# Kernel tuning notes

Measured on AMD Instinct MI355X. Metric: run time of the kernel, lower is better.

Reference implementation:

```python
import jax, jax.numpy as jnp
import numpy as np

EMBED, HEADS, FF, WIN = 512, 8, 2048, 64
SIGMA, PSTRENGTH, PERIOD, THRESH = 2.0, 1.0, 100.0, 0.0


def layer_norm(x, g, b, eps=1e-5):
    mu = jnp.mean(x, axis=-1, keepdims=True)
    var = jnp.var(x, axis=-1, keepdims=True)
    return (x - mu) * jax.lax.rsqrt(var + eps) * g + b


def setup_inputs() -> dict:
    key = jax.random.key(0)
    ks = jax.random.split(key, 16)
    s = 1.0 / np.sqrt(EMBED)
    sf = 1.0 / np.sqrt(FF)
    inp = {
        "src": jax.random.normal(ks[0], (8, 2048, EMBED), dtype=jnp.float32),
        "Wq": jax.random.normal(ks[1], (EMBED, EMBED), dtype=jnp.float32) * s,
        "bq": jnp.zeros((EMBED,), jnp.float32),
        "Wk": jax.random.normal(ks[2], (EMBED, EMBED), dtype=jnp.float32) * s,
        "bk": jnp.zeros((EMBED,), jnp.float32),
        "Wv": jax.random.normal(ks[3], (EMBED, EMBED), dtype=jnp.float32) * s,
        "bv": jnp.zeros((EMBED,), jnp.float32),
        "Wo": jax.random.normal(ks[4], (EMBED, EMBED), dtype=jnp.float32) * s,
        "bo": jnp.zeros((EMBED,), jnp.float32),
        "Wg": jax.random.normal(ks[5], (EMBED, 1), dtype=jnp.float32) * s,
        "bg": jnp.zeros((1,), jnp.float32),
        "W1": jax.random.normal(ks[6], (EMBED, FF), dtype=jnp.float32) * s,
        "b1": jnp.zeros((FF,), jnp.float32),
        "W2": jax.random.normal(ks[7], (FF, EMBED), dtype=jnp.float32) * sf,
        "b2": jnp.zeros((EMBED,), jnp.float32),
        "ln1_g": jnp.ones((EMBED,), jnp.float32),
        "ln1_b": jnp.zeros((EMBED,), jnp.float32),
        "ln2_g": jnp.ones((EMBED,), jnp.float32),
        "ln2_b": jnp.zeros((EMBED,), jnp.float32),
    }
    return inp


def gated_sparse_attn(x, Wq, bq, Wk, bk, Wv, bv, Wo, bo, Wg, bg):
    B, S, D = x.shape
    H, dh = HEADS, D // HEADS
    q = (x @ Wq + bq).reshape(B, S, H, dh).transpose(0, 2, 1, 3)  # [B,H,S,dh]
    k = (x @ Wk + bk).reshape(B, S, H, dh).transpose(0, 2, 1, 3)
    v = (x @ Wv + bv).reshape(B, S, H, dh).transpose(0, 2, 1, 3)
    scores = jnp.einsum('bhqd,bhkd->bhqk', q, k) / jnp.sqrt(jnp.float32(dh))
    idx = jnp.arange(S, dtype=jnp.float32)
    dist = idx[:, None] - idx[None, :]  # [S,S]
    gauss_bias = jnp.exp(-(dist * dist) / (2.0 * SIGMA * SIGMA))
    per_bias = PSTRENGTH * jnp.cos(2.0 * jnp.pi * dist / PERIOD)
    scores = scores + gauss_bias + per_bias  # positional biases baked into scores
    local = jnp.abs(dist) <= WIN  # local-window sparsity mask
    scores = jnp.where(local, scores, jnp.float32(-1e9))
    attn = jax.nn.softmax(scores, axis=-1)
    out = jnp.einsum('bhqk,bhkd->bhqd', attn, v)
    out = out.transpose(0, 2, 1, 3).reshape(B, S, D) @ Wo + bo
    gate = jax.nn.sigmoid(x @ Wg + bg)  # [B,S,1] learned gating
    gate = jnp.where(gate > THRESH, gate, jnp.float32(0.0))
    return gate * out


def reference(src, Wq, bq, Wk, bk, Wv, bv, Wo, bo, Wg, bg, W1, b1, W2, b2, ln1_g, ln1_b, ln2_g, ln2_b):
    # dropout is identity in eval mode
    attn_out = gated_sparse_attn(src, Wq, bq, Wk, bk, Wv, bv, Wo, bo, Wg, bg)
    x = layer_norm(src + attn_out, ln1_g, ln1_b)
    ff = jax.nn.relu(x @ W1 + b1) @ W2 + b2
    return layer_norm(x + ff, ln2_g, ln2_b)
```

## Files before the change

### kernel.cpp

```cpp
#include <hip/hip_runtime.h>
#include <hip/hip_bf16.h>
#include <math.h>

#define S_LEN   2048
#define D_MOD   512
#define N_HEADS 8
#define D_HEAD  64
#define FF_DIM  2048
#define M_ROWS  16384
#define BHSD    8388608

typedef __attribute__((ext_vector_type(8))) __bf16 bf16x8;
typedef __attribute__((ext_vector_type(4))) float  f32x4;
typedef unsigned short u16;

__device__ __forceinline__ u16 f2bf(float f) {
  unsigned u = __float_as_uint(f);
  u += 0x7fffu + ((u >> 16) & 1u);
  return (u16)(u >> 16);
}
__device__ __forceinline__ float bf2f(u16 h) { return __uint_as_float(((unsigned)h) << 16); }

__device__ __forceinline__ f32x4 mfma16(bf16x8 a, bf16x8 b, f32x4 c) {
  return __builtin_amdgcn_mfma_f32_16x16x32_bf16(a, b, c, 0, 0, 0);
}

__device__ __forceinline__ void async16(void* lds, const void* g) {
  __builtin_amdgcn_global_load_lds(
      (const __attribute__((address_space(1))) unsigned int*)g,
      (__attribute__((address_space(3))) unsigned int*)lds, 16, 0, 0);
}

#define BAR()    asm volatile("s_barrier" ::: "memory")
#define WAITV(n) asm volatile("s_waitcnt vmcnt(" #n ")" ::: "memory")
#define WAITL()  asm volatile("s_waitcnt lgkmcnt(0)" ::: "memory")

__device__ __forceinline__ int swz384(int row, int bir) {
  return row * 384 + ((bir & ~127) | ((bir ^ ((row & 7) << 4)) & 127));
}

__global__ __launch_bounds__(256) void cvt_gate(const float* __restrict__ src,
                                                const float* __restrict__ Wg,
                                                const float* __restrict__ bg,
                                                u16* __restrict__ xb,
                                                float* __restrict__ gate) {
  const int wid = threadIdx.x >> 6, lane = threadIdx.x & 63;
  const size_t row = (size_t)blockIdx.x * 4 + wid;
  const float4* s = reinterpret_cast<const float4*>(src + row * D_MOD);
  const float4* w = reinterpret_cast<const float4*>(Wg);
  float4 a0 = s[lane * 2], a1 = s[lane * 2 + 1];
  float4 w0 = w[lane * 2], w1 = w[lane * 2 + 1];
  float acc = a0.x * w0.x + a0.y * w0.y + a0.z * w0.z + a0.w * w0.w +
              a1.x * w1.x + a1.y * w1.y + a1.z * w1.z + a1.w * w1.w;
#pragma unroll
  for (int m = 1; m < 64; m <<= 1) acc += __shfl_xor(acc, m);
  ushort4 h0, h1;
  h0.x = f2bf(a0.x); h0.y = f2bf(a0.y); h0.z = f2bf(a0.z); h0.w = f2bf(a0.w);
  h1.x = f2bf(a1.x); h1.y = f2bf(a1.y); h1.z = f2bf(a1.z); h1.w = f2bf(a1.w);
  ushort4* ob = reinterpret_cast<ushort4*>(xb + row * D_MOD);
  ob[lane * 2] = h0; ob[lane * 2 + 1] = h1;
  if (lane == 0) {
    float g = 1.f / (1.f + __expf(-(acc + bg[0])));
    gate[row] = g > 0.f ? g : 0.f;
  }
}

__global__ void transpose_cvt(const float* __restrict__ in, u16* __restrict__ out,
                              int K, int N) {
  __shared__ float t[32][33];
  const int n0 = blockIdx.x * 32, k0 = blockIdx.y * 32;
  const int tx = threadIdx.x, ty = threadIdx.y;
#pragma unroll
  for (int i = 0; i < 4; ++i)
    t[ty + 8 * i][tx] = in[(size_t)(k0 + ty + 8 * i) * N + n0 + tx];
  __syncthreads();
#pragma unroll
  for (int i = 0; i < 4; ++i)
    out[(size_t)(n0 + ty + 8 * i) * K + k0 + tx] = f2bf(t[tx][ty + 8 * i]);
}

__global__ __launch_bounds__(256) void vtr_k(const u16* __restrict__ V,
                                             u16* __restrict__ VT) {
  __shared__ __align__(16) u16 T[64 * 64];
  const int tid = threadIdx.x;
  const int wid = tid >> 6, lane = tid & 63;
  const int bh = blockIdx.y;
  const int s0 = blockIdx.x * 64;
  const u16* Vb = V + ((size_t)bh * S_LEN + s0) * D_HEAD;
#pragma unroll
  for (int r = 0; r < 2; ++r) {
    const int c = r * 256 + tid;
    const int s = c >> 3;
    const int blk = (c & 7) ^ ((s >> 3) & 7);
    async16((char*)T + (r * 4 + wid) * 1024, Vb + (size_t)s * D_HEAD + blk * 8);
  }
  __syncthreads();
  u16* VTb = VT + (size_t)bh * D_HEAD * S_LEN;
#pragma unroll
  for (int r = 0; r < 2; ++r) {
    const int d  = (r * 4 + wid) * 8 + (lane >> 3);
    const int s8 = lane & 7;
    ushort4 w0, w1;
    u16 tmp[8];
#pragma unroll
    for (int j = 0; j < 8; ++j) {
      const int s = s8 * 8 + j;
      tmp[j] = *reinterpret_cast<const u16*>(
          (const char*)T + s * 128 + ((2 * d) ^ (((s >> 3) & 7) << 4)));
    }
    w0.x = tmp[0]; w0.y = tmp[1]; w0.z = tmp[2]; w0.w = tmp[3];
    w1.x = tmp[4]; w1.y = tmp[5]; w1.z = tmp[6]; w1.w = tmp[7];
    ushort4* dst = reinterpret_cast<ushort4*>(VTb + (size_t)d * S_LEN + s0 + s8 * 8);
    dst[0] = w0; dst[1] = w1;
  }
}

__global__ __launch_bounds__(256) void ln1red_k(const u16* __restrict__ xb,
                                                const float* __restrict__ gate,
                                                const u16* __restrict__ p0,
                                                const u16* __restrict__ p1,
                                                const float* __restrict__ bo,
                                                const float* __restrict__ gam,
                                                const float* __restrict__ bet,
                                                u16* __restrict__ outb) {
  const int wid = threadIdx.x >> 6, lane = threadIdx.x & 63;
  const size_t row = (size_t)blockIdx.x * 4 + wid;
  const size_t base = row * D_MOD;
  const float g = gate[row];
  const ushort4* sp = reinterpret_cast<const ushort4*>(xb + base);
  const ushort4* a  = reinterpret_cast<const ushort4*>(p0 + base);
  const ushort4* c  = reinterpret_cast<const ushort4*>(p1 + base);
  const float4*  bb = reinterpret_cast<const float4*>(bo);
  ushort4 s0 = sp[lane * 2], s1 = sp[lane * 2 + 1];
  ushort4 a0 = a[lane * 2], a1 = a[lane * 2 + 1];
  ushort4 c0 = c[lane * 2], c1 = c[lane * 2 + 1];
  float4 d0 = bb[lane * 2], d1 = bb[lane * 2 + 1];
  float4 v0, v1;
  v0.x = bf2f(s0.x) + g * (bf2f(a0.x) + bf2f(c0.x) + d0.x);
  v0.y = bf2f(s0.y) + g * (bf2f(a0.y) + bf2f(c0.y) + d0.y);
  v0.z = bf2f(s0.z) + g * (bf2f(a0.z) + bf2f(c0.z) + d0.z);
  v0.w = bf2f(s0.w) + g * (bf2f(a0.w) + bf2f(c0.w) + d0.w);
  v1.x = bf2f(s1.x) + g * (bf2f(a1.x) + bf2f(c1.x) + d1.x);
  v1.y = bf2f(s1.y) + g * (bf2f(a1.y) + bf2f(c1.y) + d1.y);
  v1.z = bf2f(s1.z) + g * (bf2f(a1.z) + bf2f(c1.z) + d1.z);
  v1.w = bf2f(s1.w) + g * (bf2f(a1.w) + bf2f(c1.w) + d1.w);
  float s  = v0.x + v0.y + v0.z + v0.w + v1.x + v1.y + v1.z + v1.w;
  float s2 = v0.x * v0.x + v0.y * v0.y + v0.z * v0.z + v0.w * v0.w +
             v1.x * v1.x + v1.y * v1.y + v1.z * v1.z + v1.w * v1.w;
#pragma unroll
  for (int m = 1; m < 64; m <<= 1) { s += __shfl_xor(s, m); s2 += __shfl_xor(s2, m); }
  const float mu = s * (1.0f / 512.0f);
  const float var = s2 * (1.0f / 512.0f) - mu * mu;
  const float rs = 1.0f / sqrtf(var + 1e-5f);
  const float4* gp = reinterpret_cast<const float4*>(gam);
  const float4* bp = reinterpret_cast<const float4*>(bet);
  float4 g0 = gp[lane * 2], g1 = gp[lane * 2 + 1];
  float4 e0 = bp[lane * 2], e1 = bp[lane * 2 + 1];
  ushort4 h0, h1;
  h0.x = f2bf((v0.x - mu) * rs * g0.x + e0.x);  h0.y = f2bf((v0.y - mu) * rs * g0.y + e0.y);
  h0.z = f2bf((v0.z - mu) * rs * g0.z + e0.z);  h0.w = f2bf((v0.w - mu) * rs * g0.w + e0.w);
  h1.x = f2bf((v1.x - mu) * rs * g1.x + e1.x);  h1.y = f2bf((v1.y - mu) * rs * g1.y + e1.y);
  h1.z = f2bf((v1.z - mu) * rs * g1.z + e1.z);  h1.w = f2bf((v1.w - mu) * rs * g1.w + e1.w);
  ushort4* ob = reinterpret_cast<ushort4*>(outb + base);
  ob[lane * 2] = h0; ob[lane * 2 + 1] = h1;
}

__global__ __launch_bounds__(256) void ln2red_k(const u16* __restrict__ xb,
                                                const u16* __restrict__ p0,
                                                const u16* __restrict__ p1,
                                                const float* __restrict__ b2,
                                                const float* __restrict__ gam,
                                                const float* __restrict__ bet,
                                                float* __restrict__ out) {
  const int wid = threadIdx.x >> 6, lane = threadIdx.x & 63;
  const size_t row = (size_t)blockIdx.x * 4 + wid;
  const size_t base = row * D_MOD;
  const ushort4* xp = reinterpret_cast<const ushort4*>(xb + base);
  const ushort4* q0 = reinterpret_cast<const ushort4*>(p0 + base);
  const ushort4* q1 = reinterpret_cast<const ushort4*>(p1 + base);
  const float4* bb = reinterpret_cast<const float4*>(b2);
  ushort4 h0 = xp[lane * 2], h1 = xp[lane * 2 + 1];
  ushort4 a0 = q0[lane * 2], a1 = q0[lane * 2 + 1];
  ushort4 c0 = q1[lane * 2], c1 = q1[lane * 2 + 1];
  float4 d0 = bb[lane * 2], d1 = bb[lane * 2 + 1];
  float4 v0, v1;
  v0.x = bf2f(h0.x) + bf2f(a0.x) + bf2f(c0.x) + d0.x;
  v0.y = bf2f(h0.y) + bf2f(a0.y) + bf2f(c0.y) + d0.y;
  v0.z = bf2f(h0.z) + bf2f(a0.z) + bf2f(c0.z) + d0.z;
  v0.w = bf2f(h0.w) + bf2f(a0.w) + bf2f(c0.w) + d0.w;
  v1.x = bf2f(h1.x) + bf2f(a1.x) + bf2f(c1.x) + d1.x;
  v1.y = bf2f(h1.y) + bf2f(a1.y) + bf2f(c1.y) + d1.y;
  v1.z = bf2f(h1.z) + bf2f(a1.z) + bf2f(c1.z) + d1.z;
  v1.w = bf2f(h1.w) + bf2f(a1.w) + bf2f(c1.w) + d1.w;
  float s  = v0.x + v0.y + v0.z + v0.w + v1.x + v1.y + v1.z + v1.w;
  float s2 = v0.x * v0.x + v0.y * v0.y + v0.z * v0.z + v0.w * v0.w +
             v1.x * v1.x + v1.y * v1.y + v1.z * v1.z + v1.w * v1.w;
#pragma unroll
  for (int m = 1; m < 64; m <<= 1) { s += __shfl_xor(s, m); s2 += __shfl_xor(s2, m); }
  const float mu = s * (1.0f / 512.0f);
  const float var = s2 * (1.0f / 512.0f) - mu * mu;
  const float rs = 1.0f / sqrtf(var + 1e-5f);
  const float4* gp = reinterpret_cast<const float4*>(gam);
  const float4* bp = reinterpret_cast<const float4*>(bet);
  float4 g0 = gp[lane * 2], g1 = gp[lane * 2 + 1];
  float4 e0 = bp[lane * 2], e1 = bp[lane * 2 + 1];
  float4 o0, o1;
  o0.x = (v0.x - mu) * rs * g0.x + e0.x;  o0.y = (v0.y - mu) * rs * g0.y + e0.y;
  o0.z = (v0.z - mu) * rs * g0.z + e0.z;  o0.w = (v0.w - mu) * rs * g0.w + e0.w;
  o1.x = (v1.x - mu) * rs * g1.x + e1.x;  o1.y = (v1.y - mu) * rs * g1.y + e1.y;
  o1.z = (v1.z - mu) * rs * g1.z + e1.z;  o1.w = (v1.w - mu) * rs * g1.w + e1.w;
  float4* q = reinterpret_cast<float4*>(out + base);
  q[lane * 2] = o0; q[lane * 2 + 1] = o1;
}

struct EpiArgs {
  const float* b0; const float* b1; const float* b2;
  float* outf; u16* outb; u16* outb2;
};

template<int EPI, int LD, int NT, int KSLICE, int GX, int GY>
__device__ __forceinline__ void gemm256_body(const u16* __restrict__ A,
                                             const u16* __restrict__ Bt, EpiArgs e) {
  extern __shared__ char smem[];
  char* Asb = smem;
  char* Bsb = smem + 65536;
  const int tid = threadIdx.x;
  const int wid = tid >> 6, lane = tid & 63;
  const int sub = lane >> 4, lc = lane & 15;
  const int wr = wid >> 2, wcn = wid & 3;

  const int nwg = (int)(gridDim.x * gridDim.y * gridDim.z);
  const int orig = ((int)blockIdx.z * (int)gridDim.y + (int)blockIdx.y) * (int)gridDim.x + (int)blockIdx.x;
  const int cpx = nwg >> 3;
  const int wg = (orig & 7) * cpx + (orig >> 3);
  const int bx = wg % GX;
  const int by = (wg / GX) % GY;
  const int bz = wg / (GX * GY);
  const int m0 = by * 256, n0 = bx * 256;
  const int kb = KSLICE * bz;

  const u16* Ab = A + (size_t)m0 * LD;
  const u16* Bb = Bt + (size_t)n0 * LD;

  f32x4 acc[8][4];
#pragma unroll
  for (int i = 0; i < 8; ++i)
#pragma unroll
    for (int j = 0; j < 4; ++j) acc[i][j] = (f32x4){0.f, 0.f, 0.f, 0.f};

  const int lr0 = tid >> 3;
  const int sl  = tid & 7;

#define STAGE(BASE, SRC, BUF, KT)                                              \
  {                                                                            \
    const int kk_ = kb + (KT) * 64;                                            \
    _Pragma("unroll")                                                          \
    for (int r_ = 0; r_ < 4; ++r_) {                                           \
      const int lr_ = r_ * 64 + lr0;                                           \
      async16((BASE) + (BUF) * 32768 + r_ * 8192 + wid * 1024,                 \
              (SRC) + (size_t)lr_ * LD + kk_ + ((sl ^ (lr_ & 7)) << 3));       \
    }                                                                          \
  }
#define LDFRAG(BASE, ROW, KS) \
  (*reinterpret_cast<const bf16x8*>((BASE) + (ROW) * 128 + ((((KS) * 64) + sub * 16) ^ (((ROW) & 7) << 4))))

  STAGE(Bsb, Bb, 0, 0);
  STAGE(Asb, Ab, 0, 0);
  STAGE(Bsb, Bb, 1, 1);
  STAGE(Asb, Ab, 1, 1);
  WAITV(8);
  BAR();

  for (int t = 0; t < NT; ++t) {
    const int buf = t & 1;
    char* Abl = Asb + buf * 32768;
    char* Bbl = Bsb + buf * 32768;
    bf16x8 af[4][2], bfr[2][2][2];
#pragma unroll
    for (int f = 0; f < 4; ++f) {
      const int row = wr * 128 + f * 16 + lc;
#pragma unroll
      for (int ks = 0; ks < 2; ++ks) af[f][ks] = LDFRAG(Abl, row, ks);
    }
#pragma unroll
    for (int f = 0; f < 2; ++f) {
      const int row = wcn * 64 + f * 16 + lc;
#pragma unroll
      for (int ks = 0; ks < 2; ++ks) bfr[0][f][ks] = LDFRAG(Bbl, row, ks);
    }
    __builtin_amdgcn_s_setprio(1);
#pragma unroll
    for (int f = 0; f < 4; ++f)
#pragma unroll
      for (int c = 0; c < 2; ++c)
#pragma unroll
        for (int ks = 0; ks < 2; ++ks)
          acc[f][c] = mfma16(af[f][ks], bfr[0][c][ks], acc[f][c]);
    __builtin_amdgcn_s_setprio(0);
    BAR();
#pragma unroll
    for (int f = 0; f < 2; ++f) {
      const int row = wcn * 64 + 32 + f * 16 + lc;
#pragma unroll
      for (int ks = 0; ks < 2; ++ks) bfr[1][f][ks] = LDFRAG(Bbl, row, ks);
    }
    __builtin_amdgcn_s_setprio(1);
#pragma unroll
    for (int f = 0; f < 4; ++f)
#pragma unroll
      for (int c = 0; c < 2; ++c)
#pragma unroll
        for (int ks = 0; ks < 2; ++ks)
          acc[f][2 + c] = mfma16(af[f][ks], bfr[1][c][ks], acc[f][2 + c]);
    __builtin_amdgcn_s_setprio(0);
    WAITL();
    BAR();
    if (t + 2 < NT) STAGE(Bsb, Bb, buf, t + 2);
#pragma unroll
    for (int f = 0; f < 4; ++f) {
      const int row = wr * 128 + 64 + f * 16 + lc;
#pragma unroll
      for (int ks = 0; ks < 2; ++ks) af[f][ks] = LDFRAG(Abl, row, ks);
    }
    __builtin_amdgcn_s_setprio(1);
#pragma unroll
    for (int f = 0; f < 4; ++f)
#pragma unroll
      for (int c = 0; c < 2; ++c)
#pragma unroll
        for (int ks = 0; ks < 2; ++ks)
          acc[4 + f][2 + c] = mfma16(af[f][ks], bfr[1][c][ks], acc[4 + f][2 + c]);
    __builtin_amdgcn_s_setprio(0);
    WAITL();
    BAR();
    if (t + 2 < NT) STAGE(Asb, Ab, buf, t + 2);
    __builtin_amdgcn_s_setprio(1);
#pragma unroll
    for (int f = 0; f < 4; ++f)
#pragma unroll
      for (int c = 0; c < 2; ++c)
#pragma unroll
        for (int ks = 0; ks < 2; ++ks)
          acc[4 + f][c] = mfma16(af[f][ks], bfr[0][c][ks], acc[4 + f][c]);
    __builtin_amdgcn_s_setprio(0);
    if (t + 1 < NT) {
      if (t + 2 < NT) { WAITV(8); } else { WAITV(0); }
      BAR();
    }
  }
#undef STAGE
#undef LDFRAG

#pragma unroll
  for (int fr = 0; fr < 8; ++fr) {
    const int row0 = m0 + wr * 128 + fr * 16 + sub * 4;
#pragma unroll
    for (int fc = 0; fc < 4; ++fc) {
      const int col = n0 + wcn * 64 + fc * 16 + lc;
      f32x4 v = acc[fr][fc];
#pragma unroll
      for (int i = 0; i < 4; ++i) {
        const int row = row0 + i;
        const float val = v[i];
        if constexpr (EPI == 0) {
          const int which = col >> 9, nn = col & 511;
          const int hh = nn >> 6, dd = nn & 63;
          const float* bp = (which == 0) ? e.b0 : (which == 1) ? e.b1 : e.b2;
          const int bb = row >> 11, ss = row & 2047;
          e.outb[(size_t)which * BHSD + (((size_t)bb * N_HEADS + hh) * S_LEN + ss) * D_HEAD + dd]
              = f2bf(val + bp[nn]);
        } else if constexpr (EPI == 2) {
          float o = val + e.b0[col];
          e.outb[(size_t)row * FF_DIM + col] = f2bf(o > 0.f ? o : 0.f);
        } else {
          u16* dst = (bz == 0) ? e.outb : e.outb2;
          dst[(size_t)row * D_MOD + col] = f2bf(val);
        }
      }
    }
  }
}

__global__ __launch_bounds__(512, 2) void k_qkv(const u16* __restrict__ A, const u16* __restrict__ B, EpiArgs e) {
  gemm256_body<0, 512, 8, 0, 6, 64>(A, B, e);
}
__global__ __launch_bounds__(512, 2) void k_ff1(const u16* __restrict__ A, const u16* __restrict__ B, EpiArgs e) {
  gemm256_body<2, 512, 8, 0, 8, 64>(A, B, e);
}
__global__ __launch_bounds__(512, 2) void k_ff2(const u16* __restrict__ A, const u16* __restrict__ B, EpiArgs e) {
  gemm256_body<4, 2048, 16, 1024, 2, 64>(A, B, e);
}
__global__ __launch_bounds__(512, 2) void k_proj(const u16* __restrict__ A, const u16* __restrict__ B, EpiArgs e) {
  gemm256_body<4, 512, 4, 256, 2, 64>(A, B, e);
}

__global__ __launch_bounds__(256)
void attn_k(const u16* __restrict__ Q, const u16* __restrict__ Kt,
            const u16* __restrict__ VTg, u16* __restrict__ Oflat) {
  __shared__ __align__(16) u16 VT[64 * 192];
  __shared__ __align__(16) u16 P [64 * 192];
  __shared__ float tab[256];
  const int tid = threadIdx.x;
  const int wid = tid >> 6, lane = tid & 63;
  const int sub = lane >> 4, lc = lane & 15;
  const int qb = blockIdx.x, bh = blockIdx.y;
  const int bb = bh >> 3, hh = bh & 7;
  const int q0 = qb * 64, kstart = q0 - 64;
  const u16* Qb = Q  + (size_t)bh * S_LEN * D_HEAD;
  const u16* Kb = Kt + (size_t)bh * S_LEN * D_HEAD;
  const u16* Vtb = VTg + (size_t)bh * D_HEAD * S_LEN;

#pragma unroll
  for (int it = 0; it < 6; ++it) {
    const int c = (wid * 6 + it) * 64 + lane;
    const int row = c / 24;
    const int bir = (c % 24) * 16;
    const int swz = (bir & ~127) | ((bir ^ ((row & 7) << 4)) & 127);
    int sb = kstart + (swz >> 1);
    sb = sb < 0 ? 0 : (sb > S_LEN - 8 ? S_LEN - 8 : sb);
    async16((char*)VT + (wid * 6 + it) * 1024, Vtb + (size_t)row * S_LEN + sb);
  }

  if (tid < 255) {
    const int di = tid - 127;
    const float fd = (float)di;
    tab[tid] = (di >= -64 && di <= 64)
        ? __expf(-fd * fd * 0.125f) + __cosf(0.06283185307179586f * fd)
        : -1e9f;
  }

  bf16x8 qf[2];
#pragma unroll
  for (int ks = 0; ks < 2; ++ks)
    qf[ks] = *reinterpret_cast<const bf16x8*>(Qb + (size_t)(q0 + wid * 16 + lc) * D_HEAD + ks * 32 + sub * 8);

  f32x4 sc[12];
#pragma unroll
  for (int t = 0; t < 12; ++t) sc[t] = (f32x4){0.f, 0.f, 0.f, 0.f};
#pragma unroll
  for (int ks = 0; ks < 2; ++ks)
#pragma unroll
    for (int t = 0; t < 12; ++t) {
      int kg = kstart + t * 16 + lc;
      int kc = kg < 0 ? 0 : (kg > S_LEN - 1 ? S_LEN - 1 : kg);
      bf16x8 kf = *reinterpret_cast<const bf16x8*>(Kb + (size_t)kc * D_HEAD + ks * 32 + sub * 8);
      sc[t] = mfma16(qf[ks], kf, sc[t]);
    }
  __syncthreads();

  float rmax[4] = {-3e38f, -3e38f, -3e38f, -3e38f};
#pragma unroll
  for (int t = 0; t < 12; ++t) {
    const int kk = t * 16 + lc;
    const int kg = kstart + kk;
    const bool valid = (kg >= 0) && (kg < S_LEN);
#pragma unroll
    for (int r = 0; r < 4; ++r) {
      const int qrow = wid * 16 + sub * 4 + r;
      const float bias = valid ? tab[qrow - kk + 191] : -1e9f;
      const float sv = sc[t][r] * 0.125f + bias;
      sc[t][r] = sv;
      rmax[r] = fmaxf(rmax[r], sv);
    }
  }
#pragma unroll
  for (int m = 1; m < 16; m <<= 1)
#pragma unroll
    for (int r = 0; r < 4; ++r) rmax[r] = fmaxf(rmax[r], __shfl_xor(rmax[r], m));
  float rsum[4] = {0.f, 0.f, 0.f, 0.f};
#pragma unroll
  for (int t = 0; t < 12; ++t)
#pragma unroll
    for (int r = 0; r < 4; ++r) {
      const float p = __expf(sc[t][r] - rmax[r]);
      sc[t][r] = p; rsum[r] += p;
    }
#pragma unroll
  for (int m = 1; m < 16; m <<= 1)
#pragma unroll
    for (int r = 0; r < 4; ++r) rsum[r] += __shfl_xor(rsum[r], m);
  float rinv[4];
#pragma unroll
  for (int r = 0; r < 4; ++r) rinv[r] = 1.0f / rsum[r];
#pragma unroll
  for (int t = 0; t < 12; ++t)
#pragma unroll
    for (int r = 0; r < 4; ++r) {
      const int qrow = wid * 16 + sub * 4 + r;
      *reinterpret_cast<u16*>(reinterpret_cast<char*>(P) + swz384(qrow, (t * 16 + lc) * 2))
          = f2bf(sc[t][r] * rinv[r]);
    }
  __syncthreads();

  f32x4 oacc[4];
#pragma unroll
  for (int t = 0; t < 4; ++t) oacc[t] = (f32x4){0.f, 0.f, 0.f, 0.f};
  const int arow = wid * 16 + lc;
#pragma unroll
  for (int ks = 0; ks < 6; ++ks) {
    const int bir = ks * 64 + sub * 16;
    bf16x8 pa = *reinterpret_cast<const bf16x8*>(reinterpret_cast<char*>(P) + swz384(arow, bir));
#pragma unroll
    for (int t = 0; t < 4; ++t) {
      bf16x8 vb = *reinterpret_cast<const bf16x8*>(reinterpret_cast<char*>(VT) + swz384(t * 16 + lc, bir));
      oacc[t] = mfma16(pa, vb, oacc[t]);
    }
  }

  const size_t obase = ((size_t)bb * S_LEN + q0) * D_MOD + hh * D_HEAD;
#pragma unroll
  for (int t = 0; t < 4; ++t)
#pragma unroll
    for (int r = 0; r < 4; ++r) {
      const int qrow = wid * 16 + sub * 4 + r;
      Oflat[obase + (size_t)qrow * D_MOD + t * 16 + lc] = f2bf(oacc[t][r]);
    }
}

extern "C" void kernel_launch(void* const* d_in, const int* in_sizes, int n_in,
                              void* d_out, int out_size, void* d_ws, size_t ws_size,
                              hipStream_t stream) {
  (void)in_sizes; (void)n_in; (void)out_size; (void)ws_size;
  const float* src  = (const float*)d_in[0];
  const float* Wq   = (const float*)d_in[1];
  const float* bq   = (const float*)d_in[2];
  const float* Wk   = (const float*)d_in[3];
  const float* bk   = (const float*)d_in[4];
  const float* Wv   = (const float*)d_in[5];
  const float* bv   = (const float*)d_in[6];
  const float* Wo   = (const float*)d_in[7];
  const float* bo   = (const float*)d_in[8];
  const float* Wg   = (const float*)d_in[9];
  const float* bg   = (const float*)d_in[10];
  const float* W1   = (const float*)d_in[11];
  const float* b1   = (const float*)d_in[12];
  const float* W2   = (const float*)d_in[13];
  const float* b2   = (const float*)d_in[14];
  const float* ln1g = (const float*)d_in[15];
  const float* ln1b = (const float*)d_in[16];
  const float* ln2g = (const float*)d_in[17];
  const float* ln2b = (const float*)d_in[18];
  float* out = (float*)d_out;

  char* ws = (char*)d_ws;
  u16*   WqkvT  = (u16*)  (ws + 0);
  u16*   WoT    = (u16*)  (ws + 1572864);
  u16*   W1T    = (u16*)  (ws + 2097152);
  u16*   W2T    = (u16*)  (ws + 4194304);
  float* gatef  = (float*)(ws + 6291456);
  u16*   Xbf    = (u16*)  (ws + 6356992);
  u16*   QKVbf  = (u16*)  (ws + 23134208);
  u16*   attnfl = (u16*)  (ws + 73465856);
  u16*   pr0    = (u16*)  (ws + 90243072);
  u16*   pr1    = (u16*)  (ws + 107020288);
  u16*   xbf2   = (u16*)  (ws + 123797504);
  u16*   VTg    = (u16*)  (ws + 140574720);
  u16*   hbuf   = Xbf;
  u16*   pf0    = pr0;
  u16*   pf1    = pr1;

  (void)hipFuncSetAttribute((const void*)k_qkv,  hipFuncAttributeMaxDynamicSharedMemorySize, 131072);
  (void)hipFuncSetAttribute((const void*)k_ff1,  hipFuncAttributeMaxDynamicSharedMemorySize, 131072);
  (void)hipFuncSetAttribute((const void*)k_ff2,  hipFuncAttributeMaxDynamicSharedMemorySize, 131072);
  (void)hipFuncSetAttribute((const void*)k_proj, hipFuncAttributeMaxDynamicSharedMemorySize, 131072);

  dim3 tb(32, 8);
  cvt_gate<<<4096, 256, 0, stream>>>(src, Wg, bg, Xbf, gatef);
  transpose_cvt<<<dim3(16, 16), tb, 0, stream>>>(Wq, WqkvT,             512, 512);
  transpose_cvt<<<dim3(16, 16), tb, 0, stream>>>(Wk, WqkvT + 512 * 512, 512, 512);
  transpose_cvt<<<dim3(16, 16), tb, 0, stream>>>(Wv, WqkvT + 2 * 512 * 512, 512, 512);
  transpose_cvt<<<dim3(16, 16), tb, 0, stream>>>(Wo, WoT, 512, 512);
  transpose_cvt<<<dim3(64, 16), tb, 0, stream>>>(W1, W1T, 512, 2048);
  transpose_cvt<<<dim3(16, 64), tb, 0, stream>>>(W2, W2T, 2048, 512);

  EpiArgs e1{bq, bk, bv, nullptr, QKVbf, nullptr};
  k_qkv<<<dim3(6, 64, 1), 512, 131072, stream>>>(Xbf, WqkvT, e1);

  vtr_k<<<dim3(32, 64), 256, 0, stream>>>(QKVbf + 2 * BHSD, VTg);

  attn_k<<<dim3(32, 64), 256, 0, stream>>>(QKVbf, QKVbf + BHSD, VTg, attnfl);

  EpiArgs e2{nullptr, nullptr, nullptr, nullptr, pr0, pr1};
  k_proj<<<dim3(2, 64, 2), 512, 131072, stream>>>(attnfl, WoT, e2);

  ln1red_k<<<4096, 256, 0, stream>>>(Xbf, gatef, pr0, pr1, bo, ln1g, ln1b, xbf2);

  EpiArgs e3{b1, nullptr, nullptr, nullptr, hbuf, nullptr};
  k_ff1<<<dim3(8, 64, 1), 512, 131072, stream>>>(xbf2, W1T, e3);

  EpiArgs e4{nullptr, nullptr, nullptr, nullptr, pf0, pf1};
  k_ff2<<<dim3(2, 64, 2), 512, 131072, stream>>>(hbuf, W2T, e4);

  ln2red_k<<<4096, 256, 0, stream>>>(xbf2, pf0, pf1, b2, ln2g, ln2b, out);
}
```

Baseline: 223.4 us.

## Fuse V transpose into QKV GEMM epilogue and stage FF/proj stores via LDS

The QKV GEMM epilogue now writes the V slice directly in transposed [B,H,D,S] layout as 4-wide vector stores, which removes the separate vtr_k kernel and its extra read and write of V. The FF1, FF2 and projection epilogues now stage the bf16 results in swizzled shared memory and then write them out as coalesced 16-byte row stores instead of scattered 2-byte stores. The cost is two extra barriers and LDS traffic in those epilogues. The transposed V stores are also strided across S rows.

Result: slower. 230.6 us (+3.2%).

```diff
diff --git a/kernel.cpp b/kernel.cpp
--- a/kernel.cpp
+++ b/kernel.cpp
@@ -77,42 +77,6 @@
 #pragma unroll
   for (int i = 0; i < 4; ++i)
     out[(size_t)(n0 + ty + 8 * i) * K + k0 + tx] = f2bf(t[tx][ty + 8 * i]);
-}
-
-__global__ __launch_bounds__(256) void vtr_k(const u16* __restrict__ V,
-                                             u16* __restrict__ VT) {
-  __shared__ __align__(16) u16 T[64 * 64];
-  const int tid = threadIdx.x;
-  const int wid = tid >> 6, lane = tid & 63;
-  const int bh = blockIdx.y;
-  const int s0 = blockIdx.x * 64;
-  const u16* Vb = V + ((size_t)bh * S_LEN + s0) * D_HEAD;
-#pragma unroll
-  for (int r = 0; r < 2; ++r) {
-    const int c = r * 256 + tid;
-    const int s = c >> 3;
-    const int blk = (c & 7) ^ ((s >> 3) & 7);
-    async16((char*)T + (r * 4 + wid) * 1024, Vb + (size_t)s * D_HEAD + blk * 8);
-  }
-  __syncthreads();
-  u16* VTb = VT + (size_t)bh * D_HEAD * S_LEN;
-#pragma unroll
-  for (int r = 0; r < 2; ++r) {
-    const int d  = (r * 4 + wid) * 8 + (lane >> 3);
-    const int s8 = lane & 7;
-    ushort4 w0, w1;
-    u16 tmp[8];
-#pragma unroll
-    for (int j = 0; j < 8; ++j) {
-      const int s = s8 * 8 + j;
-      tmp[j] = *reinterpret_cast<const u16*>(
-          (const char*)T + s * 128 + ((2 * d) ^ (((s >> 3) & 7) << 4)));
-    }
-    w0.x = tmp[0]; w0.y = tmp[1]; w0.z = tmp[2]; w0.w = tmp[3];
-    w1.x = tmp[4]; w1.y = tmp[5]; w1.z = tmp[6]; w1.w = tmp[7];
-    ushort4* dst = reinterpret_cast<ushort4*>(VTb + (size_t)d * S_LEN + s0 + s8 * 8);
-    dst[0] = w0; dst[1] = w1;
-  }
 }
 
 __global__ __launch_bounds__(256) void ln1red_k(const u16* __restrict__ xb,
@@ -351,30 +315,68 @@
 #undef STAGE
 #undef LDFRAG
 
-#pragma unroll
-  for (int fr = 0; fr < 8; ++fr) {
-    const int row0 = m0 + wr * 128 + fr * 16 + sub * 4;
-#pragma unroll
-    for (int fc = 0; fc < 4; ++fc) {
-      const int col = n0 + wcn * 64 + fc * 16 + lc;
-      f32x4 v = acc[fr][fc];
-#pragma unroll
-      for (int i = 0; i < 4; ++i) {
-        const int row = row0 + i;
-        const float val = v[i];
-        if constexpr (EPI == 0) {
-          const int which = col >> 9, nn = col & 511;
-          const int hh = nn >> 6, dd = nn & 63;
-          const float* bp = (which == 0) ? e.b0 : (which == 1) ? e.b1 : e.b2;
-          const int bb = row >> 11, ss = row & 2047;
-          e.outb[(size_t)which * BHSD + (((size_t)bb * N_HEADS + hh) * S_LEN + ss) * D_HEAD + dd]
-              = f2bf(val + bp[nn]);
-        } else if constexpr (EPI == 2) {
-          float o = val + e.b0[col];
-          e.outb[(size_t)row * FF_DIM + col] = f2bf(o > 0.f ? o : 0.f);
+  if constexpr (EPI == 2 || EPI == 4) {
+    __syncthreads();
+    u16* Cs = reinterpret_cast<u16*>(smem);
+#pragma unroll
+    for (int fr = 0; fr < 8; ++fr) {
+      const int lrow = wr * 128 + fr * 16 + sub * 4;
+#pragma unroll
+      for (int fc = 0; fc < 4; ++fc) {
+        const int lcolb = (wcn * 64 + fc * 16 + lc) * 2;
+        float bias = 0.f;
+        if constexpr (EPI == 2) bias = e.b0[n0 + wcn * 64 + fc * 16 + lc];
+        f32x4 v = acc[fr][fc];
+#pragma unroll
+        for (int i = 0; i < 4; ++i) {
+          float o = v[i] + bias;
+          u16 hv;
+          if constexpr (EPI == 2) hv = f2bf(o > 0.f ? o : 0.f);
+          else                    hv = f2bf(o);
+          const int row = lrow + i;
+          const int cbs = (lcolb & ~127) | ((lcolb ^ ((row & 7) << 4)) & 127);
+          *reinterpret_cast<u16*>((char*)Cs + row * 512 + cbs) = hv;
+        }
+      }
+    }
+    __syncthreads();
+    u16* dstb;
+    size_t pitch;
+    if constexpr (EPI == 2) { dstb = e.outb; pitch = FF_DIM; }
+    else { dstb = (bz == 0) ? e.outb : e.outb2; pitch = D_MOD; }
+#pragma unroll
+    for (int p = 0; p < 16; ++p) {
+      const int off = p * 8192 + tid * 16;
+      const int row = off >> 9, cb = off & 511;
+      const int cbs = (cb & ~127) | ((cb ^ ((row & 7) << 4)) & 127);
+      uint4 v = *reinterpret_cast<const uint4*>((const char*)Cs + row * 512 + cbs);
+      *reinterpret_cast<uint4*>((char*)(dstb + (size_t)(m0 + row) * pitch + n0) + cb) = v;
+    }
+  } else {
+#pragma unroll
+    for (int fr = 0; fr < 8; ++fr) {
+      const int row0 = m0 + wr * 128 + fr * 16 + sub * 4;
+      const int bbi = row0 >> 11, ss = row0 & 2047;
+#pragma unroll
+      for (int fc = 0; fc < 4; ++fc) {
+        const int col = n0 + wcn * 64 + fc * 16 + lc;
+        const int which = col >> 9, nn = col & 511;
+        const int hh = nn >> 6, dd = nn & 63;
+        const float* bp = (which == 0) ? e.b0 : (which == 1) ? e.b1 : e.b2;
+        const float bias = bp[nn];
+        f32x4 v = acc[fr][fc];
+        if (which == 2) {
+          ushort4 h;
+          h.x = f2bf(v[0] + bias); h.y = f2bf(v[1] + bias);
+          h.z = f2bf(v[2] + bias); h.w = f2bf(v[3] + bias);
+          *reinterpret_cast<ushort4*>(
+              e.outb2 + (((size_t)bbi * N_HEADS + hh) * D_HEAD + dd) * S_LEN + ss) = h;
         } else {
-          u16* dst = (bz == 0) ? e.outb : e.outb2;
-          dst[(size_t)row * D_MOD + col] = f2bf(val);
+#pragma unroll
+          for (int i = 0; i < 4; ++i)
+            e.outb[(size_t)which * BHSD +
+                   (((size_t)bbi * N_HEADS + hh) * S_LEN + ss + i) * D_HEAD + dd]
+                = f2bf(v[i] + bias);
         }
       }
     }
@@ -573,10 +575,8 @@
   transpose_cvt<<<dim3(64, 16), tb, 0, stream>>>(W1, W1T, 512, 2048);
   transpose_cvt<<<dim3(16, 64), tb, 0, stream>>>(W2, W2T, 2048, 512);
 
-  EpiArgs e1{bq, bk, bv, nullptr, QKVbf, nullptr};
+  EpiArgs e1{bq, bk, bv, nullptr, QKVbf, VTg};
   k_qkv<<<dim3(6, 64, 1), 512, 131072, stream>>>(Xbf, WqkvT, e1);
-
-  vtr_k<<<dim3(32, 64), 256, 0, stream>>>(QKVbf + 2 * BHSD, VTg);
 
   attn_k<<<dim3(32, 64), 256, 0, stream>>>(QKVbf, QKVbf + BHSD, VTg, attnfl);
 
```
